# Performance work log

Measured on AMD Instinct MI355X. Metric: run time of the kernel, lower is better.

Reference implementation:

```python
import jax, jax.numpy as jnp
import numpy as np

NUM_HEADS = 8
NUM_GROUPS = 32
EPS = 1e-5


def setup_inputs() -> dict:
    key = jax.random.key(0)
    ks = jax.random.split(key, 7)
    B, C, H, W = 8, 512, 32, 32
    x = jax.random.normal(ks[0], (B, C, H, W), dtype=jnp.float32)
    # GroupNorm affine params
    gn_w = jnp.ones((C,), dtype=jnp.float32)
    gn_b = jnp.zeros((C,), dtype=jnp.float32)
    # 1x1 conv == linear over channel dim; store squeezed weights (out, in)
    qkv_w = jax.random.normal(ks[1], (3 * C, C), dtype=jnp.float32) * (1.0 / np.sqrt(C))
    qkv_b = jnp.zeros((3 * C,), dtype=jnp.float32)
    proj_w = jax.random.normal(ks[2], (C, C), dtype=jnp.float32) * (1.0 / np.sqrt(C))
    proj_b = jnp.zeros((C,), dtype=jnp.float32)
    return {"x": x, "gn_w": gn_w, "gn_b": gn_b, "qkv_w": qkv_w,
            "qkv_b": qkv_b, "proj_w": proj_w, "proj_b": proj_b}


def reference(x, gn_w, gn_b, qkv_w, qkv_b, proj_w, proj_b):
    B, C, H, W = x.shape
    G = NUM_GROUPS
    hd = C // NUM_HEADS
    scale = hd ** -0.5
    # GroupNorm: normalize over (C//G, H, W) per group
    xg = x.reshape(B, G, C // G, H, W)
    mean = xg.mean(axis=(2, 3, 4), keepdims=True)
    var = xg.var(axis=(2, 3, 4), keepdims=True)
    xn = ((xg - mean) * jax.lax.rsqrt(var + EPS)).reshape(B, C, H, W)
    xn = xn * gn_w[None, :, None, None] + gn_b[None, :, None, None]
    # QKV 1x1 conv
    qkv = jnp.einsum('bchw,oc->bohw', xn, qkv_w) + qkv_b[None, :, None, None]
    # (B, 3, heads, head_dim, HW) -> (3, B, heads, HW, head_dim)
    qkv = qkv.reshape(B, 3, NUM_HEADS, hd, H * W).transpose(1, 0, 2, 4, 3)
    q, k, v = qkv[0], qkv[1], qkv[2]
    attn = jax.nn.softmax(jnp.einsum('bhqd,bhkd->bhqk', q, k) * scale, axis=-1)
    out = jnp.einsum('bhqk,bhkd->bhqd', attn, v)  # (B, heads, HW, hd)
    out = out.transpose(0, 1, 3, 2).reshape(B, C, H, W)
    out = jnp.einsum('bchw,oc->bohw', out, proj_w) + proj_b[None, :, None, None]
    return out + x
```

## Files before the change

kernel.cpp:

```cpp
#include <hip/hip_runtime.h>
#include <hip/hip_bf16.h>
#include <math.h>

typedef __bf16 bf16_t;
typedef __bf16 bf16x8 __attribute__((ext_vector_type(8)));
typedef __bf16 bf16x4 __attribute__((ext_vector_type(4)));
typedef float  f32x4  __attribute__((ext_vector_type(4)));
typedef short  short4v __attribute__((ext_vector_type(4)));

#define NB    8
#define NC    512
#define NHW   1024
#define NHEAD 8
#define NHD   64
#define NG    32
#define NCG   16
#define NO3   1536

__device__ __forceinline__ void lds_load16(bf16_t* lds, const bf16_t* g) {
  __builtin_amdgcn_global_load_lds(
      (__attribute__((address_space(1))) unsigned int*)(g),
      (__attribute__((address_space(3))) unsigned int*)(void*)(lds),
      16, 0, 0);
}

__device__ __forceinline__ f32x4 mfma16(bf16x4 a, bf16x4 b, f32x4 c) {
#if __has_builtin(__builtin_amdgcn_mfma_f32_16x16x16bf16_1k)
  return __builtin_amdgcn_mfma_f32_16x16x16bf16_1k(
      __builtin_bit_cast(short4v, a), __builtin_bit_cast(short4v, b), c, 0, 0, 0);
#else
  f32x4 d;
  asm("v_mfma_f32_16x16x16_bf16 %0, %1, %2, %3"
      : "=v"(d) : "v"(a), "v"(b), "v"(c));
  return d;
#endif
}

__global__ __launch_bounds__(256)
void gn_kernel(const float* __restrict__ x, const float* __restrict__ gw,
               const float* __restrict__ gb, bf16_t* __restrict__ xn)
{
  const int bg = blockIdx.x;
  const int b = bg >> 5, g = bg & 31;
  const float* xp = x + ((size_t)b * NC + g * NCG) * NHW;
  const int tid = threadIdx.x;
  const int wave = tid >> 6, lane = tid & 63;

  float s1 = 0.f, s2 = 0.f;
  const float4* xp4 = (const float4*)xp;
  for (int i = tid; i < 4096; i += 256) {
    float4 v = xp4[i];
    s1 += v.x + v.y + v.z + v.w;
    s2 += v.x * v.x + v.y * v.y + v.z * v.z + v.w * v.w;
  }
  for (int off = 32; off > 0; off >>= 1) {
    s1 += __shfl_down(s1, off);
    s2 += __shfl_down(s2, off);
  }
  __shared__ float red[16];
  if (lane == 0) { red[wave] = s1; red[8 + wave] = s2; }
  __syncthreads();
  float tot1 = red[0] + red[1] + red[2] + red[3];
  float tot2 = red[8] + red[9] + red[10] + red[11];
  const float mean = tot1 * (1.0f / 16384.0f);
  const float var  = tot2 * (1.0f / 16384.0f) - mean * mean;
  const float rstd = rsqrtf(var + 1e-5f);

  float gam[NCG], bet[NCG];
  #pragma unroll
  for (int c = 0; c < NCG; ++c) {
    gam[c] = gw[g * NCG + c] * rstd;
    bet[c] = gb[g * NCG + c] - mean * gam[c];
  }
  bf16_t* op = xn + (size_t)b * NHW * NC + g * NCG;
  for (int s = tid; s < NHW; s += 256) {
    __align__(16) bf16_t vals[NCG];
    #pragma unroll
    for (int c = 0; c < NCG; ++c)
      vals[c] = (bf16_t)(xp[c * NHW + s] * gam[c] + bet[c]);
    *(bf16x8*)(op + (size_t)s * NC)     = *(const bf16x8*)&vals[0];
    *(bf16x8*)(op + (size_t)s * NC + 8) = *(const bf16x8*)&vals[8];
  }
}

__global__ __launch_bounds__(256)
void wconv_kernel(const float* __restrict__ qw, const float* __restrict__ pw,
                  bf16_t* __restrict__ qwb, bf16_t* __restrict__ pwb)
{
  const int gid = blockIdx.x * 256 + threadIdx.x;
  const int n1 = NO3 * NC / 4;
  float4 v; bf16x4 o;
  if (gid < n1) {
    v = ((const float4*)qw)[gid];
    o[0] = (bf16_t)v.x; o[1] = (bf16_t)v.y; o[2] = (bf16_t)v.z; o[3] = (bf16_t)v.w;
    ((bf16x4*)qwb)[gid] = o;
  } else {
    int g2 = gid - n1;
    v = ((const float4*)pw)[g2];
    o[0] = (bf16_t)v.x; o[1] = (bf16_t)v.y; o[2] = (bf16_t)v.z; o[3] = (bf16_t)v.w;
    ((bf16x4*)pwb)[g2] = o;
  }
}

__device__ __forceinline__ void gemm_mainloop(const bf16_t* Ap, const bf16_t* Bp,
                                              bf16_t* sA, bf16_t* sB, f32x4 (&acc)[4][4])
{
  const int tid = threadIdx.x;
  const int wave = tid >> 6, lane = tid & 63;
  const int quad = lane >> 4, l16 = lane & 15;
  const int wm = wave >> 1, wn = wave & 1;
  for (int k0 = 0; k0 < 512; k0 += 32) {
    #pragma unroll
    for (int j = 0; j < 2; ++j) {
      int c = wave * 64 + j * 256 + lane;
      int row = c >> 2, ko = (c & 3) * 8;
      lds_load16(sA + (size_t)(wave * 64 + j * 256) * 8, Ap + (size_t)row * 512 + k0 + ko);
      lds_load16(sB + (size_t)(wave * 64 + j * 256) * 8, Bp + (size_t)row * 512 + k0 + ko);
    }
    __syncthreads();
    bf16x8 af[4], bfr[4];
    #pragma unroll
    for (int mi = 0; mi < 4; ++mi)
      af[mi] = *(const bf16x8*)(sA + (wm * 64 + mi * 16 + l16) * 32 + quad * 8);
    #pragma unroll
    for (int ni = 0; ni < 4; ++ni)
      bfr[ni] = *(const bf16x8*)(sB + (wn * 64 + ni * 16 + l16) * 32 + quad * 8);
    #pragma unroll
    for (int mi = 0; mi < 4; ++mi)
      #pragma unroll
      for (int ni = 0; ni < 4; ++ni)
        acc[mi][ni] = __builtin_amdgcn_mfma_f32_16x16x32_bf16(af[mi], bfr[ni], acc[mi][ni], 0, 0, 0);
    __syncthreads();
  }
}

__global__ __launch_bounds__(256, 2)
void qkv_gemm(const bf16_t* __restrict__ xn, const bf16_t* __restrict__ w,
              const float* __restrict__ bias,
              bf16_t* __restrict__ qbuf, bf16_t* __restrict__ kbuf, bf16_t* __restrict__ vbuf)
{
  __shared__ __align__(16) bf16_t smem[128 * 136];
  bf16_t* sA = smem;
  bf16_t* sB = smem + 4096;
  const int tid = threadIdx.x;
  const int wave = tid >> 6, lane = tid & 63;
  const int quad = lane >> 4, l16 = lane & 15;
  const int wm = wave >> 1, wn = wave & 1;
  const int bx = blockIdx.x, by = blockIdx.y, b = blockIdx.z;

  const bf16_t* Ap = xn + ((size_t)b * NHW + by * 128) * NC;
  const bf16_t* Bp = w + (size_t)bx * 128 * NC;
  f32x4 acc[4][4] = {};
  gemm_mainloop(Ap, Bp, sA, sB, acc);

  const int obase = bx * 128 + wn * 64;
  const int sbase = by * 128 + wm * 64;
  float bv[4];
  #pragma unroll
  for (int ni = 0; ni < 4; ++ni) bv[ni] = bias[obase + ni * 16 + l16];

  if (bx < 8) {
    const bool isq = (bx < 4);
    bf16_t* basep = isq ? qbuf : kbuf;
    const float scale = isq ? 0.125f : 1.0f;
    #pragma unroll
    for (int ni = 0; ni < 4; ++ni) {
      int o = obase + ni * 16 + l16;
      int hh = (o >> 6) & 7, dd = o & 63;
      bf16_t* dst = basep + ((size_t)(b * NHEAD + hh) * NHW) * NHD + dd;
      #pragma unroll
      for (int mi = 0; mi < 4; ++mi)
        #pragma unroll
        for (int r = 0; r < 4; ++r) {
          int s = sbase + mi * 16 + quad * 4 + r;
          dst[(size_t)s * NHD] = (bf16_t)((acc[mi][ni][r] + bv[ni]) * scale);
        }
    }
  } else {
    bf16_t* sC = smem;
    __syncthreads();
    #pragma unroll
    for (int ni = 0; ni < 4; ++ni)
      #pragma unroll
      for (int mi = 0; mi < 4; ++mi)
        #pragma unroll
        for (int r = 0; r < 4; ++r)
          sC[(wn * 64 + ni * 16 + l16) * 136 + wm * 64 + mi * 16 + quad * 4 + r] =
              (bf16_t)(acc[mi][ni][r] + bv[ni]);
    __syncthreads();
    int o_local = tid >> 1, shalf = (tid & 1) << 6;
    int ov = (bx - 8) * 128 + o_local;
    int hh = ov >> 6, dd = ov & 63;
    bf16_t* dst = vbuf + ((size_t)(b * NHEAD + hh) * NHD + dd) * NHW + by * 128 + shalf;
    #pragma unroll
    for (int jj = 0; jj < 8; ++jj)
      *(bf16x8*)(dst + jj * 8) = *(const bf16x8*)&sC[o_local * 136 + shalf + jj * 8];
  }
}

__global__ __launch_bounds__(256, 2)
void attn_kernel(const bf16_t* __restrict__ qbuf, const bf16_t* __restrict__ kbuf,
                 const bf16_t* __restrict__ vbuf, bf16_t* __restrict__ obuf)
{
  __shared__ __align__(16) bf16_t Ks[128 * 72];
  __shared__ __align__(16) bf16_t Vs[64 * 136];

  const int tid = threadIdx.x;
  const int wave = tid >> 6, lane = tid & 63;
  const int quad = lane >> 4, l16 = lane & 15;
  const int idx = blockIdx.x;
  const int qt = idx & 7, h = (idx >> 3) & 7, b = idx >> 6;
  const size_t bh = (size_t)b * NHEAD + h;
  const bf16_t* qp = qbuf + (bh * NHW + qt * 128 + wave * 32) * NHD;
  const bf16_t* kp = kbuf + bh * NHW * NHD;
  const bf16_t* vp = vbuf + bh * NHD * NHW;

  bf16x8 qf[2][2];
  #pragma unroll
  for (int stile = 0; stile < 2; ++stile)
    #pragma unroll
    for (int kc = 0; kc < 2; ++kc)
      qf[stile][kc] = *(const bf16x8*)(qp + (size_t)(stile * 16 + l16) * NHD + kc * 32 + quad * 8);

  float m_i[2] = {-1e30f, -1e30f}, l_i[2] = {0.f, 0.f};
  f32x4 oacc[4][2] = {};

  for (int kt = 0; kt < 8; ++kt) {
    const bf16_t* ksrc = kp + (size_t)kt * 128 * NHD;
    const bf16_t* vsrc = vp + kt * 128;
    #pragma unroll
    for (int j = 0; j < 4; ++j) {
      int c = tid + j * 256;
      int t = c >> 3, doff = (c & 7) * 8;
      *(bf16x8*)&Ks[t * 72 + doff] = *(const bf16x8*)(ksrc + (size_t)t * NHD + doff);
    }
    #pragma unroll
    for (int j = 0; j < 4; ++j) {
      int c = tid + j * 256;
      int d = c >> 4, toff = (c & 15) * 8;
      *(bf16x8*)&Vs[d * 136 + toff] = *(const bf16x8*)(vsrc + (size_t)d * NHW + toff);
    }
    __syncthreads();

    f32x4 st[2][8];
    #pragma unroll
    for (int mt = 0; mt < 8; ++mt) {
      bf16x8 ka0 = *(const bf16x8*)&Ks[(mt * 16 + l16) * 72 + quad * 8];
      bf16x8 ka1 = *(const bf16x8*)&Ks[(mt * 16 + l16) * 72 + 32 + quad * 8];
      #pragma unroll
      for (int stile = 0; stile < 2; ++stile) {
        f32x4 z = {};
        z = __builtin_amdgcn_mfma_f32_16x16x32_bf16(ka0, qf[stile][0], z, 0, 0, 0);
        z = __builtin_amdgcn_mfma_f32_16x16x32_bf16(ka1, qf[stile][1], z, 0, 0, 0);
        st[stile][mt] = z;
      }
    }

    #pragma unroll
    for (int stile = 0; stile < 2; ++stile) {
      float mx = -1e30f;
      #pragma unroll
      for (int mt = 0; mt < 8; ++mt)
        #pragma unroll
        for (int r = 0; r < 4; ++r) mx = fmaxf(mx, st[stile][mt][r]);
      mx = fmaxf(mx, __shfl_xor(mx, 16));
      mx = fmaxf(mx, __shfl_xor(mx, 32));
      float mnew = fmaxf(m_i[stile], mx);
      float alpha = __expf(m_i[stile] - mnew);
      m_i[stile] = mnew;
      float rs = 0.f;
      #pragma unroll
      for (int mt = 0; mt < 8; ++mt)
        #pragma unroll
        for (int r = 0; r < 4; ++r) {
          float p = __expf(st[stile][mt][r] - mnew);
          rs += p;
          st[stile][mt][r] = p;
        }
      rs += __shfl_xor(rs, 16);
      rs += __shfl_xor(rs, 32);
      l_i[stile] = l_i[stile] * alpha + rs;
      #pragma unroll
      for (int mi = 0; mi < 4; ++mi)
        #pragma unroll
        for (int r = 0; r < 4; ++r)
          oacc[mi][stile][r] *= alpha;
    }

    #pragma unroll
    for (int mt = 0; mt < 8; ++mt) {
      bf16x4 pb[2];
      #pragma unroll
      for (int stile = 0; stile < 2; ++stile) {
        pb[stile][0] = (bf16_t)st[stile][mt][0];
        pb[stile][1] = (bf16_t)st[stile][mt][1];
        pb[stile][2] = (bf16_t)st[stile][mt][2];
        pb[stile][3] = (bf16_t)st[stile][mt][3];
      }
      #pragma unroll
      for (int mi = 0; mi < 4; ++mi) {
        bf16x4 va = *(const bf16x4*)&Vs[(mi * 16 + l16) * 136 + mt * 16 + quad * 4];
        oacc[mi][0] = mfma16(va, pb[0], oacc[mi][0]);
        oacc[mi][1] = mfma16(va, pb[1], oacc[mi][1]);
      }
    }
    __syncthreads();
  }

  #pragma unroll
  for (int stile = 0; stile < 2; ++stile) {
    float inv = 1.0f / l_i[stile];
    int s = qt * 128 + wave * 32 + stile * 16 + l16;
    bf16_t* orow = obuf + ((size_t)b * NHW + s) * NC + h * NHD;
    #pragma unroll
    for (int mi = 0; mi < 4; ++mi) {
      __align__(8) bf16_t o4[4];
      #pragma unroll
      for (int r = 0; r < 4; ++r) o4[r] = (bf16_t)(oacc[mi][stile][r] * inv);
      *(bf16x4*)(orow + mi * 16 + quad * 4) = *(const bf16x4*)o4;
    }
  }
}

__global__ __launch_bounds__(256, 2)
void proj_gemm(const bf16_t* __restrict__ ob, const bf16_t* __restrict__ w,
               const float* __restrict__ bias, const float* __restrict__ x,
               float* __restrict__ out)
{
  __shared__ __align__(16) bf16_t smem[8192];
  bf16_t* sA = smem;
  bf16_t* sB = smem + 4096;
  const int tid = threadIdx.x;
  const int wave = tid >> 6, lane = tid & 63;
  const int quad = lane >> 4, l16 = lane & 15;
  const int wm = wave >> 1, wn = wave & 1;
  const int bx = blockIdx.x, by = blockIdx.y, b = blockIdx.z;

  const bf16_t* Ap = w + (size_t)by * 128 * NC;
  const bf16_t* Bp = ob + ((size_t)b * NHW + bx * 128) * NC;
  f32x4 acc[4][4] = {};
  gemm_mainloop(Ap, Bp, sA, sB, acc);

  const int cobase = by * 128 + wm * 64;
  const int sbase  = bx * 128 + wn * 64;
  #pragma unroll
  for (int mi = 0; mi < 4; ++mi)
    #pragma unroll
    for (int r = 0; r < 4; ++r) {
      int co = cobase + mi * 16 + quad * 4 + r;
      float pb = bias[co];
      const float* xrow = x + ((size_t)b * NC + co) * NHW;
      float* orow = out + ((size_t)b * NC + co) * NHW;
      #pragma unroll
      for (int ni = 0; ni < 4; ++ni) {
        int s = sbase + ni * 16 + l16;
        orow[s] = acc[mi][ni][r] + pb + xrow[s];
      }
    }
}

extern "C" void kernel_launch(void* const* d_in, const int* in_sizes, int n_in,
                              void* d_out, int out_size, void* d_ws, size_t ws_size,
                              hipStream_t stream)
{
  const float* x      = (const float*)d_in[0];
  const float* gn_w   = (const float*)d_in[1];
  const float* gn_b   = (const float*)d_in[2];
  const float* qkv_w  = (const float*)d_in[3];
  const float* qkv_b  = (const float*)d_in[4];
  const float* proj_w = (const float*)d_in[5];
  const float* proj_b = (const float*)d_in[6];
  float* out = (float*)d_out;

  char* ws = (char*)d_ws;
  bf16_t* xn   = (bf16_t*)(ws);
  bf16_t* qwb  = (bf16_t*)(ws + 8388608);
  bf16_t* pwb  = (bf16_t*)(ws + 9961472);
  bf16_t* qbuf = (bf16_t*)(ws + 10485760);
  bf16_t* kbuf = (bf16_t*)(ws + 18874368);
  bf16_t* vbuf = (bf16_t*)(ws + 27262976);
  bf16_t* obuf = xn;

  gn_kernel<<<dim3(NB * NG), dim3(256), 0, stream>>>(x, gn_w, gn_b, xn);
  wconv_kernel<<<dim3(1024), dim3(256), 0, stream>>>(qkv_w, proj_w, qwb, pwb);
  qkv_gemm<<<dim3(12, 8, NB), dim3(256), 0, stream>>>(xn, qwb, qkv_b, qbuf, kbuf, vbuf);
  attn_kernel<<<dim3(512), dim3(256), 0, stream>>>(qbuf, kbuf, vbuf, obuf);
  proj_gemm<<<dim3(8, 4, NB), dim3(256), 0, stream>>>(obuf, pwb, proj_b, x, out);
}
```

Before: 172.4 us.

## Deepen GEMM K-step, stage Q/K stores via LDS, split attention into smaller query tiles

The shared GEMM mainloop now loads a 64-wide K slab (two 32-wide halves) per barrier pair, halving the number of synchronizations. The Q/K epilogue of the QKV GEMM is staged through LDS so each thread writes contiguous 16-byte vectors instead of scattered 2-byte stores. The attention kernel uses 64-query blocks with one 16-row tile per wave, launching twice as many blocks with a higher occupancy bound. Softmax switches to exp2 with log2e folded into the Q scale. Each K/V tile is now loaded by twice as many blocks, and the GEMMs use more LDS per block.

```diff
diff --git a/kernel.cpp b/kernel.cpp
--- a/kernel.cpp
+++ b/kernel.cpp
@@ -16,6 +16,7 @@
 #define NG    32
 #define NCG   16
 #define NO3   1536
+#define LOG2E 1.4426950408889634f
 
 __device__ __forceinline__ void lds_load16(bf16_t* lds, const bf16_t* g) {
   __builtin_amdgcn_global_load_lds(
@@ -109,27 +110,35 @@
   const int wave = tid >> 6, lane = tid & 63;
   const int quad = lane >> 4, l16 = lane & 15;
   const int wm = wave >> 1, wn = wave & 1;
-  for (int k0 = 0; k0 < 512; k0 += 32) {
-    #pragma unroll
-    for (int j = 0; j < 2; ++j) {
-      int c = wave * 64 + j * 256 + lane;
-      int row = c >> 2, ko = (c & 3) * 8;
-      lds_load16(sA + (size_t)(wave * 64 + j * 256) * 8, Ap + (size_t)row * 512 + k0 + ko);
-      lds_load16(sB + (size_t)(wave * 64 + j * 256) * 8, Bp + (size_t)row * 512 + k0 + ko);
-    }
-    __syncthreads();
-    bf16x8 af[4], bfr[4];
-    #pragma unroll
-    for (int mi = 0; mi < 4; ++mi)
-      af[mi] = *(const bf16x8*)(sA + (wm * 64 + mi * 16 + l16) * 32 + quad * 8);
-    #pragma unroll
-    for (int ni = 0; ni < 4; ++ni)
-      bfr[ni] = *(const bf16x8*)(sB + (wn * 64 + ni * 16 + l16) * 32 + quad * 8);
-    #pragma unroll
-    for (int mi = 0; mi < 4; ++mi)
+  for (int k0 = 0; k0 < 512; k0 += 64) {
+    #pragma unroll
+    for (int half = 0; half < 2; ++half) {
+      #pragma unroll
+      for (int j = 0; j < 2; ++j) {
+        int c = wave * 64 + j * 256 + lane;
+        int row = c >> 2, ko = (c & 3) * 8;
+        lds_load16(sA + half * 4096 + (size_t)(wave * 64 + j * 256) * 8,
+                   Ap + (size_t)row * 512 + k0 + half * 32 + ko);
+        lds_load16(sB + half * 4096 + (size_t)(wave * 64 + j * 256) * 8,
+                   Bp + (size_t)row * 512 + k0 + half * 32 + ko);
+      }
+    }
+    __syncthreads();
+    #pragma unroll
+    for (int half = 0; half < 2; ++half) {
+      bf16x8 af[4], bfr[4];
+      #pragma unroll
+      for (int mi = 0; mi < 4; ++mi)
+        af[mi] = *(const bf16x8*)(sA + half * 4096 + (wm * 64 + mi * 16 + l16) * 32 + quad * 8);
       #pragma unroll
       for (int ni = 0; ni < 4; ++ni)
-        acc[mi][ni] = __builtin_amdgcn_mfma_f32_16x16x32_bf16(af[mi], bfr[ni], acc[mi][ni], 0, 0, 0);
+        bfr[ni] = *(const bf16x8*)(sB + half * 4096 + (wn * 64 + ni * 16 + l16) * 32 + quad * 8);
+      #pragma unroll
+      for (int mi = 0; mi < 4; ++mi)
+        #pragma unroll
+        for (int ni = 0; ni < 4; ++ni)
+          acc[mi][ni] = __builtin_amdgcn_mfma_f32_16x16x32_bf16(af[mi], bfr[ni], acc[mi][ni], 0, 0, 0);
+    }
     __syncthreads();
   }
 }
@@ -141,7 +150,7 @@
 {
   __shared__ __align__(16) bf16_t smem[128 * 136];
   bf16_t* sA = smem;
-  bf16_t* sB = smem + 4096;
+  bf16_t* sB = smem + 8192;
   const int tid = threadIdx.x;
   const int wave = tid >> 6, lane = tid & 63;
   const int quad = lane >> 4, l16 = lane & 15;
@@ -154,7 +163,6 @@
   gemm_mainloop(Ap, Bp, sA, sB, acc);
 
   const int obase = bx * 128 + wn * 64;
-  const int sbase = by * 128 + wm * 64;
   float bv[4];
   #pragma unroll
   for (int ni = 0; ni < 4; ++ni) bv[ni] = bias[obase + ni * 16 + l16];
@@ -162,20 +170,25 @@
   if (bx < 8) {
     const bool isq = (bx < 4);
     bf16_t* basep = isq ? qbuf : kbuf;
-    const float scale = isq ? 0.125f : 1.0f;
-    #pragma unroll
-    for (int ni = 0; ni < 4; ++ni) {
-      int o = obase + ni * 16 + l16;
-      int hh = (o >> 6) & 7, dd = o & 63;
-      bf16_t* dst = basep + ((size_t)(b * NHEAD + hh) * NHW) * NHD + dd;
+    const float scale = isq ? (0.125f * LOG2E) : 1.0f;
+    bf16_t* sC = smem;
+    __syncthreads();
+    #pragma unroll
+    for (int ni = 0; ni < 4; ++ni)
       #pragma unroll
       for (int mi = 0; mi < 4; ++mi)
         #pragma unroll
-        for (int r = 0; r < 4; ++r) {
-          int s = sbase + mi * 16 + quad * 4 + r;
-          dst[(size_t)s * NHD] = (bf16_t)((acc[mi][ni][r] + bv[ni]) * scale);
-        }
-    }
+        for (int r = 0; r < 4; ++r)
+          sC[(wm * 64 + mi * 16 + quad * 4 + r) * 136 + wn * 64 + ni * 16 + l16] =
+              (bf16_t)((acc[mi][ni][r] + bv[ni]) * scale);
+    __syncthreads();
+    int s_local = tid >> 1;
+    int ohalf = (tid & 1) << 6;
+    int hh = ((bx & 3) << 1) | (tid & 1);
+    bf16_t* dst = basep + (((size_t)(b * NHEAD + hh)) * NHW + by * 128 + s_local) * NHD;
+    #pragma unroll
+    for (int jj = 0; jj < 8; ++jj)
+      *(bf16x8*)(dst + jj * 8) = *(const bf16x8*)&sC[s_local * 136 + ohalf + jj * 8];
   } else {
     bf16_t* sC = smem;
     __syncthreads();
@@ -198,7 +211,7 @@
   }
 }
 
-__global__ __launch_bounds__(256, 2)
+__global__ __launch_bounds__(256, 4)
 void attn_kernel(const bf16_t* __restrict__ qbuf, const bf16_t* __restrict__ kbuf,
                  const bf16_t* __restrict__ vbuf, bf16_t* __restrict__ obuf)
 {
@@ -209,21 +222,19 @@
   const int wave = tid >> 6, lane = tid & 63;
   const int quad = lane >> 4, l16 = lane & 15;
   const int idx = blockIdx.x;
-  const int qt = idx & 7, h = (idx >> 3) & 7, b = idx >> 6;
+  const int qt = idx & 15, h = (idx >> 4) & 7, b = idx >> 7;
   const size_t bh = (size_t)b * NHEAD + h;
-  const bf16_t* qp = qbuf + (bh * NHW + qt * 128 + wave * 32) * NHD;
+  const bf16_t* qp = qbuf + (bh * NHW + qt * 64 + wave * 16) * NHD;
   const bf16_t* kp = kbuf + bh * NHW * NHD;
   const bf16_t* vp = vbuf + bh * NHD * NHW;
 
-  bf16x8 qf[2][2];
-  #pragma unroll
-  for (int stile = 0; stile < 2; ++stile)
-    #pragma unroll
-    for (int kc = 0; kc < 2; ++kc)
-      qf[stile][kc] = *(const bf16x8*)(qp + (size_t)(stile * 16 + l16) * NHD + kc * 32 + quad * 8);
-
-  float m_i[2] = {-1e30f, -1e30f}, l_i[2] = {0.f, 0.f};
-  f32x4 oacc[4][2] = {};
+  bf16x8 qf[2];
+  #pragma unroll
+  for (int kc = 0; kc < 2; ++kc)
+    qf[kc] = *(const bf16x8*)(qp + (size_t)l16 * NHD + kc * 32 + quad * 8);
+
+  float m_i = -1e30f, l_i = 0.f;
+  f32x4 oacc[4] = {};
 
   for (int kt = 0; kt < 8; ++kt) {
     const bf16_t* ksrc = kp + (size_t)kt * 128 * NHD;
@@ -242,83 +253,70 @@
     }
     __syncthreads();
 
-    f32x4 st[2][8];
+    f32x4 st[8];
     #pragma unroll
     for (int mt = 0; mt < 8; ++mt) {
       bf16x8 ka0 = *(const bf16x8*)&Ks[(mt * 16 + l16) * 72 + quad * 8];
       bf16x8 ka1 = *(const bf16x8*)&Ks[(mt * 16 + l16) * 72 + 32 + quad * 8];
-      #pragma unroll
-      for (int stile = 0; stile < 2; ++stile) {
-        f32x4 z = {};
-        z = __builtin_amdgcn_mfma_f32_16x16x32_bf16(ka0, qf[stile][0], z, 0, 0, 0);
-        z = __builtin_amdgcn_mfma_f32_16x16x32_bf16(ka1, qf[stile][1], z, 0, 0, 0);
-        st[stile][mt] = z;
+      f32x4 z = {};
+      z = __builtin_amdgcn_mfma_f32_16x16x32_bf16(ka0, qf[0], z, 0, 0, 0);
+      z = __builtin_amdgcn_mfma_f32_16x16x32_bf16(ka1, qf[1], z, 0, 0, 0);
+      st[mt] = z;
+    }
+
+    float mx = -1e30f;
+    #pragma unroll
+    for (int mt = 0; mt < 8; ++mt)
+      #pragma unroll
+      for (int r = 0; r < 4; ++r) mx = fmaxf(mx, st[mt][r]);
+    mx = fmaxf(mx, __shfl_xor(mx, 16));
+    mx = fmaxf(mx, __shfl_xor(mx, 32));
+    float mnew = fmaxf(m_i, mx);
+    float alpha = exp2f(m_i - mnew);
+    m_i = mnew;
+    float rs = 0.f;
+    #pragma unroll
+    for (int mt = 0; mt < 8; ++mt)
+      #pragma unroll
+      for (int r = 0; r < 4; ++r) {
+        float p = exp2f(st[mt][r] - mnew);
+        rs += p;
+        st[mt][r] = p;
       }
-    }
-
-    #pragma unroll
-    for (int stile = 0; stile < 2; ++stile) {
-      float mx = -1e30f;
-      #pragma unroll
-      for (int mt = 0; mt < 8; ++mt)
-        #pragma unroll
-        for (int r = 0; r < 4; ++r) mx = fmaxf(mx, st[stile][mt][r]);
-      mx = fmaxf(mx, __shfl_xor(mx, 16));
-      mx = fmaxf(mx, __shfl_xor(mx, 32));
-      float mnew = fmaxf(m_i[stile], mx);
-      float alpha = __expf(m_i[stile] - mnew);
-      m_i[stile] = mnew;
-      float rs = 0.f;
-      #pragma unroll
-      for (int mt = 0; mt < 8; ++mt)
-        #pragma unroll
-        for (int r = 0; r < 4; ++r) {
-          float p = __expf(st[stile][mt][r] - mnew);
-          rs += p;
-          st[stile][mt][r] = p;
-        }
-      rs += __shfl_xor(rs, 16);
-      rs += __shfl_xor(rs, 32);
-      l_i[stile] = l_i[stile] * alpha + rs;
-      #pragma unroll
-      for (int mi = 0; mi < 4; ++mi)
-        #pragma unroll
-        for (int r = 0; r < 4; ++r)
-          oacc[mi][stile][r] *= alpha;
-    }
+    rs += __shfl_xor(rs, 16);
+    rs += __shfl_xor(rs, 32);
+    l_i = l_i * alpha + rs;
+    #pragma unroll
+    for (int mi = 0; mi < 4; ++mi)
+      #pragma unroll
+      for (int r = 0; r < 4; ++r)
+        oacc[mi][r] *= alpha;
 
     #pragma unroll
     for (int mt = 0; mt < 8; ++mt) {
-      bf16x4 pb[2];
-      #pragma unroll
-      for (int stile = 0; stile < 2; ++stile) {
-        pb[stile][0] = (bf16_t)st[stile][mt][0];
-        pb[stile][1] = (bf16_t)st[stile][mt][1];
-        pb[stile][2] = (bf16_t)st[stile][mt][2];
-        pb[stile][3] = (bf16_t)st[stile][mt][3];
-      }
+      bf16x4 pb;
+      pb[0] = (bf16_t)st[mt][0];
+      pb[1] = (bf16_t)st[mt][1];
+      pb[2] = (bf16_t)st[mt][2];
+      pb[3] = (bf16_t)st[mt][3];
       #pragma unroll
       for (int mi = 0; mi < 4; ++mi) {
         bf16x4 va = *(const bf16x4*)&Vs[(mi * 16 + l16) * 136 + mt * 16 + quad * 4];
-        oacc[mi][0] = mfma16(va, pb[0], oacc[mi][0]);
-        oacc[mi][1] = mfma16(va, pb[1], oacc[mi][1]);
+        oacc[mi] = mfma16(va, pb, oacc[mi]);
       }
     }
     __syncthreads();
   }
 
-  #pragma unroll
-  for (int stile = 0; stile < 2; ++stile) {
-    float inv = 1.0f / l_i[stile];
-    int s = qt * 128 + wave * 32 + stile * 16 + l16;
-    bf16_t* orow = obuf + ((size_t)b * NHW + s) * NC + h * NHD;
-    #pragma unroll
-    for (int mi = 0; mi < 4; ++mi) {
-      __align__(8) bf16_t o4[4];
-      #pragma unroll
-      for (int r = 0; r < 4; ++r) o4[r] = (bf16_t)(oacc[mi][stile][r] * inv);
-      *(bf16x4*)(orow + mi * 16 + quad * 4) = *(const bf16x4*)o4;
-    }
+  float inv = 1.0f / l_i;
+  int s = qt * 64 + wave * 16 + l16;
+  bf16_t* orow = obuf + ((size_t)b * NHW + s) * NC + h * NHD;
+  #pragma unroll
+  for (int mi = 0; mi < 4; ++mi) {
+    __align__(8) bf16_t o4[4];
+    #pragma unroll
+    for (int r = 0; r < 4; ++r) o4[r] = (bf16_t)(oacc[mi][r] * inv);
+    *(bf16x4*)(orow + mi * 16 + quad * 4) = *(const bf16x4*)o4;
   }
 }
 
@@ -327,9 +325,9 @@
                const float* __restrict__ bias, const float* __restrict__ x,
                float* __restrict__ out)
 {
-  __shared__ __align__(16) bf16_t smem[8192];
+  __shared__ __align__(16) bf16_t smem[16384];
   bf16_t* sA = smem;
-  bf16_t* sB = smem + 4096;
+  bf16_t* sB = smem + 8192;
   const int tid = threadIdx.x;
   const int wave = tid >> 6, lane = tid & 63;
   const int quad = lane >> 4, l16 = lane & 15;
@@ -384,6 +382,6 @@
   gn_kernel<<<dim3(NB * NG), dim3(256), 0, stream>>>(x, gn_w, gn_b, xn);
   wconv_kernel<<<dim3(1024), dim3(256), 0, stream>>>(qkv_w, proj_w, qwb, pwb);
   qkv_gemm<<<dim3(12, 8, NB), dim3(256), 0, stream>>>(xn, qwb, qkv_b, qbuf, kbuf, vbuf);
-  attn_kernel<<<dim3(512), dim3(256), 0, stream>>>(qbuf, kbuf, vbuf, obuf);
+  attn_kernel<<<dim3(1024), dim3(256), 0, stream>>>(qbuf, kbuf, vbuf, obuf);
   proj_gemm<<<dim3(8, 4, NB), dim3(256), 0, stream>>>(obuf, pwb, proj_b, x, out);
 }
```

Result: slower. 179.8 us (+4.3%).

## Split attention over key halves with combine kernel, widen GEMM K-step, stage Q/K stores

Applied to the files above, without the earlier changes.

Attention now runs twice as many blocks, each covering half of the key tiles. Each block writes unnormalized partial outputs plus running max and sum, and a new combine kernel merges the two halves. The softmax switches to exp2 with log2e folded into the Q scale. The shared GEMM mainloop loads 64-wide K slices per barrier to halve the number of synchronizations, at the cost of more LDS. Q/K writes in the QKV GEMM are staged through LDS for coalesced 16-byte stores. The split adds partial-output traffic and an extra launch, and the attention kernel drops its occupancy hint.

```diff
diff --git a/kernel.cpp b/kernel.cpp
--- a/kernel.cpp
+++ b/kernel.cpp
@@ -16,6 +16,7 @@
 #define NG    32
 #define NCG   16
 #define NO3   1536
+#define LOG2E 1.4426950408889634f
 
 __device__ __forceinline__ void lds_load16(bf16_t* lds, const bf16_t* g) {
   __builtin_amdgcn_global_load_lds(
@@ -109,27 +110,35 @@
   const int wave = tid >> 6, lane = tid & 63;
   const int quad = lane >> 4, l16 = lane & 15;
   const int wm = wave >> 1, wn = wave & 1;
-  for (int k0 = 0; k0 < 512; k0 += 32) {
-    #pragma unroll
-    for (int j = 0; j < 2; ++j) {
-      int c = wave * 64 + j * 256 + lane;
-      int row = c >> 2, ko = (c & 3) * 8;
-      lds_load16(sA + (size_t)(wave * 64 + j * 256) * 8, Ap + (size_t)row * 512 + k0 + ko);
-      lds_load16(sB + (size_t)(wave * 64 + j * 256) * 8, Bp + (size_t)row * 512 + k0 + ko);
-    }
-    __syncthreads();
-    bf16x8 af[4], bfr[4];
-    #pragma unroll
-    for (int mi = 0; mi < 4; ++mi)
-      af[mi] = *(const bf16x8*)(sA + (wm * 64 + mi * 16 + l16) * 32 + quad * 8);
-    #pragma unroll
-    for (int ni = 0; ni < 4; ++ni)
-      bfr[ni] = *(const bf16x8*)(sB + (wn * 64 + ni * 16 + l16) * 32 + quad * 8);
-    #pragma unroll
-    for (int mi = 0; mi < 4; ++mi)
+  for (int k0 = 0; k0 < 512; k0 += 64) {
+    #pragma unroll
+    for (int half = 0; half < 2; ++half) {
+      #pragma unroll
+      for (int j = 0; j < 2; ++j) {
+        int c = wave * 64 + j * 256 + lane;
+        int row = c >> 2, ko = (c & 3) * 8;
+        lds_load16(sA + half * 4096 + (size_t)(wave * 64 + j * 256) * 8,
+                   Ap + (size_t)row * 512 + k0 + half * 32 + ko);
+        lds_load16(sB + half * 4096 + (size_t)(wave * 64 + j * 256) * 8,
+                   Bp + (size_t)row * 512 + k0 + half * 32 + ko);
+      }
+    }
+    __syncthreads();
+    #pragma unroll
+    for (int half = 0; half < 2; ++half) {
+      bf16x8 af[4], bfr[4];
+      #pragma unroll
+      for (int mi = 0; mi < 4; ++mi)
+        af[mi] = *(const bf16x8*)(sA + half * 4096 + (wm * 64 + mi * 16 + l16) * 32 + quad * 8);
       #pragma unroll
       for (int ni = 0; ni < 4; ++ni)
-        acc[mi][ni] = __builtin_amdgcn_mfma_f32_16x16x32_bf16(af[mi], bfr[ni], acc[mi][ni], 0, 0, 0);
+        bfr[ni] = *(const bf16x8*)(sB + half * 4096 + (wn * 64 + ni * 16 + l16) * 32 + quad * 8);
+      #pragma unroll
+      for (int mi = 0; mi < 4; ++mi)
+        #pragma unroll
+        for (int ni = 0; ni < 4; ++ni)
+          acc[mi][ni] = __builtin_amdgcn_mfma_f32_16x16x32_bf16(af[mi], bfr[ni], acc[mi][ni], 0, 0, 0);
+    }
     __syncthreads();
   }
 }
@@ -141,7 +150,7 @@
 {
   __shared__ __align__(16) bf16_t smem[128 * 136];
   bf16_t* sA = smem;
-  bf16_t* sB = smem + 4096;
+  bf16_t* sB = smem + 8192;
   const int tid = threadIdx.x;
   const int wave = tid >> 6, lane = tid & 63;
   const int quad = lane >> 4, l16 = lane & 15;
@@ -154,7 +163,6 @@
   gemm_mainloop(Ap, Bp, sA, sB, acc);
 
   const int obase = bx * 128 + wn * 64;
-  const int sbase = by * 128 + wm * 64;
   float bv[4];
   #pragma unroll
   for (int ni = 0; ni < 4; ++ni) bv[ni] = bias[obase + ni * 16 + l16];
@@ -162,20 +170,25 @@
   if (bx < 8) {
     const bool isq = (bx < 4);
     bf16_t* basep = isq ? qbuf : kbuf;
-    const float scale = isq ? 0.125f : 1.0f;
-    #pragma unroll
-    for (int ni = 0; ni < 4; ++ni) {
-      int o = obase + ni * 16 + l16;
-      int hh = (o >> 6) & 7, dd = o & 63;
-      bf16_t* dst = basep + ((size_t)(b * NHEAD + hh) * NHW) * NHD + dd;
+    const float scale = isq ? (0.125f * LOG2E) : 1.0f;
+    bf16_t* sC = smem;
+    __syncthreads();
+    #pragma unroll
+    for (int ni = 0; ni < 4; ++ni)
       #pragma unroll
       for (int mi = 0; mi < 4; ++mi)
         #pragma unroll
-        for (int r = 0; r < 4; ++r) {
-          int s = sbase + mi * 16 + quad * 4 + r;
-          dst[(size_t)s * NHD] = (bf16_t)((acc[mi][ni][r] + bv[ni]) * scale);
-        }
-    }
+        for (int r = 0; r < 4; ++r)
+          sC[(wm * 64 + mi * 16 + quad * 4 + r) * 136 + wn * 64 + ni * 16 + l16] =
+              (bf16_t)((acc[mi][ni][r] + bv[ni]) * scale);
+    __syncthreads();
+    int s_local = tid >> 1;
+    int ohalf = (tid & 1) << 6;
+    int hh = ((bx & 3) << 1) | (tid & 1);
+    bf16_t* dst = basep + (((size_t)(b * NHEAD + hh)) * NHW + by * 128 + s_local) * NHD;
+    #pragma unroll
+    for (int jj = 0; jj < 8; ++jj)
+      *(bf16x8*)(dst + jj * 8) = *(const bf16x8*)&sC[s_local * 136 + ohalf + jj * 8];
   } else {
     bf16_t* sC = smem;
     __syncthreads();
@@ -198,9 +211,10 @@
   }
 }
 
-__global__ __launch_bounds__(256, 2)
+__global__ __launch_bounds__(256)
 void attn_kernel(const bf16_t* __restrict__ qbuf, const bf16_t* __restrict__ kbuf,
-                 const bf16_t* __restrict__ vbuf, bf16_t* __restrict__ obuf)
+                 const bf16_t* __restrict__ vbuf, bf16_t* __restrict__ Pbuf,
+                 float* __restrict__ ml)
 {
   __shared__ __align__(16) bf16_t Ks[128 * 72];
   __shared__ __align__(16) bf16_t Vs[64 * 136];
@@ -209,7 +223,9 @@
   const int wave = tid >> 6, lane = tid & 63;
   const int quad = lane >> 4, l16 = lane & 15;
   const int idx = blockIdx.x;
-  const int qt = idx & 7, h = (idx >> 3) & 7, b = idx >> 6;
+  const int qt = idx & 7, h = (idx >> 3) & 7, b = (idx >> 6) & 7;
+  const int half = idx >> 9;
+  const int p = idx & 511;
   const size_t bh = (size_t)b * NHEAD + h;
   const bf16_t* qp = qbuf + (bh * NHW + qt * 128 + wave * 32) * NHD;
   const bf16_t* kp = kbuf + bh * NHW * NHD;
@@ -225,7 +241,7 @@
   float m_i[2] = {-1e30f, -1e30f}, l_i[2] = {0.f, 0.f};
   f32x4 oacc[4][2] = {};
 
-  for (int kt = 0; kt < 8; ++kt) {
+  for (int kt = half * 4; kt < half * 4 + 4; ++kt) {
     const bf16_t* ksrc = kp + (size_t)kt * 128 * NHD;
     const bf16_t* vsrc = vp + kt * 128;
     #pragma unroll
@@ -266,16 +282,16 @@
       mx = fmaxf(mx, __shfl_xor(mx, 16));
       mx = fmaxf(mx, __shfl_xor(mx, 32));
       float mnew = fmaxf(m_i[stile], mx);
-      float alpha = __expf(m_i[stile] - mnew);
+      float alpha = exp2f(m_i[stile] - mnew);
       m_i[stile] = mnew;
       float rs = 0.f;
       #pragma unroll
       for (int mt = 0; mt < 8; ++mt)
         #pragma unroll
         for (int r = 0; r < 4; ++r) {
-          float p = __expf(st[stile][mt][r] - mnew);
-          rs += p;
-          st[stile][mt][r] = p;
+          float pv = exp2f(st[stile][mt][r] - mnew);
+          rs += pv;
+          st[stile][mt][r] = pv;
         }
       rs += __shfl_xor(rs, 16);
       rs += __shfl_xor(rs, 32);
@@ -307,18 +323,52 @@
     __syncthreads();
   }
 
+  float* mlrow = ml + (size_t)(half * 512 + p) * 256;
+  bf16_t* prow = Pbuf + (size_t)(half * 512 + p) * 128 * NHD;
   #pragma unroll
   for (int stile = 0; stile < 2; ++stile) {
-    float inv = 1.0f / l_i[stile];
-    int s = qt * 128 + wave * 32 + stile * 16 + l16;
-    bf16_t* orow = obuf + ((size_t)b * NHW + s) * NC + h * NHD;
+    int s_local = wave * 32 + stile * 16 + l16;
+    if (quad == 0) { mlrow[s_local] = m_i[stile]; mlrow[128 + s_local] = l_i[stile]; }
     #pragma unroll
     for (int mi = 0; mi < 4; ++mi) {
       __align__(8) bf16_t o4[4];
       #pragma unroll
-      for (int r = 0; r < 4; ++r) o4[r] = (bf16_t)(oacc[mi][stile][r] * inv);
-      *(bf16x4*)(orow + mi * 16 + quad * 4) = *(const bf16x4*)o4;
-    }
+      for (int r = 0; r < 4; ++r) o4[r] = (bf16_t)oacc[mi][stile][r];
+      *(bf16x4*)(prow + (size_t)s_local * NHD + mi * 16 + quad * 4) = *(const bf16x4*)o4;
+    }
+  }
+}
+
+__global__ __launch_bounds__(256)
+void combine_kernel(const bf16_t* __restrict__ Pbuf, const float* __restrict__ ml,
+                    bf16_t* __restrict__ obuf)
+{
+  const int p = blockIdx.x;
+  const int qt = p & 7, h = (p >> 3) & 7, b = (p >> 6) & 7;
+  const int tid = threadIdx.x;
+  const int s_local = tid >> 1, dh = (tid & 1) << 5;
+
+  float m0 = ml[(size_t)p * 256 + s_local];
+  float l0 = ml[(size_t)p * 256 + 128 + s_local];
+  float m1 = ml[(size_t)(512 + p) * 256 + s_local];
+  float l1 = ml[(size_t)(512 + p) * 256 + 128 + s_local];
+  float mm = fmaxf(m0, m1);
+  float a0 = exp2f(m0 - mm), a1 = exp2f(m1 - mm);
+  float inv = 1.0f / (a0 * l0 + a1 * l1);
+  a0 *= inv; a1 *= inv;
+
+  const bf16_t* r0 = Pbuf + ((size_t)p * 128 + s_local) * NHD + dh;
+  const bf16_t* r1 = Pbuf + ((size_t)(512 + p) * 128 + s_local) * NHD + dh;
+  bf16_t* o = obuf + ((size_t)b * NHW + qt * 128 + s_local) * NC + h * NHD + dh;
+  #pragma unroll
+  for (int jj = 0; jj < 4; ++jj) {
+    bf16x8 v0 = *(const bf16x8*)(r0 + jj * 8);
+    bf16x8 v1 = *(const bf16x8*)(r1 + jj * 8);
+    bf16x8 vo;
+    #pragma unroll
+    for (int e = 0; e < 8; ++e)
+      vo[e] = (bf16_t)(a0 * (float)v0[e] + a1 * (float)v1[e]);
+    *(bf16x8*)(o + jj * 8) = vo;
   }
 }
 
@@ -327,9 +377,9 @@
                const float* __restrict__ bias, const float* __restrict__ x,
                float* __restrict__ out)
 {
-  __shared__ __align__(16) bf16_t smem[8192];
+  __shared__ __align__(16) bf16_t smem[16384];
   bf16_t* sA = smem;
-  bf16_t* sB = smem + 4096;
+  bf16_t* sB = smem + 8192;
   const int tid = threadIdx.x;
   const int wave = tid >> 6, lane = tid & 63;
   const int quad = lane >> 4, l16 = lane & 15;
@@ -379,11 +429,17 @@
   bf16_t* qbuf = (bf16_t*)(ws + 10485760);
   bf16_t* kbuf = (bf16_t*)(ws + 18874368);
   bf16_t* vbuf = (bf16_t*)(ws + 27262976);
-  bf16_t* obuf = xn;
+  bf16_t* Pbuf = xn;
+  bf16_t* obuf = qbuf;
+  float*  ml   = (float*)(ws + 44040192);
+
+  Pbuf = (bf16_t*)(ws + 35651584);
+  ml   = (float*)(ws + 52428800);
 
   gn_kernel<<<dim3(NB * NG), dim3(256), 0, stream>>>(x, gn_w, gn_b, xn);
   wconv_kernel<<<dim3(1024), dim3(256), 0, stream>>>(qkv_w, proj_w, qwb, pwb);
   qkv_gemm<<<dim3(12, 8, NB), dim3(256), 0, stream>>>(xn, qwb, qkv_b, qbuf, kbuf, vbuf);
-  attn_kernel<<<dim3(512), dim3(256), 0, stream>>>(qbuf, kbuf, vbuf, obuf);
+  attn_kernel<<<dim3(1024), dim3(256), 0, stream>>>(qbuf, kbuf, vbuf, Pbuf, ml);
+  combine_kernel<<<dim3(512), dim3(256), 0, stream>>>(Pbuf, ml, obuf);
   proj_gemm<<<dim3(8, 4, NB), dim3(256), 0, stream>>>(obuf, pwb, proj_b, x, out);
 }
```

Result: slower. 198.9 us (+15.3%).
